# Kernel optimization log

Measured on AMD Instinct MI355X. Metric: run time of the kernel, lower is better.

## Reference

```python
import jax, jax.numpy as jnp
import numpy as np

D_MODEL, HEADS, GROUPS, DIM_HEAD = 256, 8, 8, 64
INNER = HEADS * DIM_HEAD              # 512
OFF_DIMS = INNER // GROUPS            # 64 channels fed to the offset network per group
DF, OFF_SCALE, KS, PAD = 4, 4.0, 6, 1  # downsample_factor, offset_scale, kernel, (6-4)//2
CPB_DIM = D_MODEL // 4                # 64
NUM_LAYERS = 6
SCALE = DIM_HEAD ** -0.5
B, H, W = 1, 40, 40


def grouped_conv1x1(x, w, g):
    # x: (b, cin, h, w); w: (cout, cin//g) torch grouped 1x1 conv weight (squeezed)
    b, cin, h, wd = x.shape
    cout = w.shape[0]
    xg = x.reshape(b, g, cin // g, h, wd)
    wg = w.reshape(g, cout // g, cin // g)
    return jnp.einsum('goi,bgihw->bgohw', wg, xg).reshape(b, cout, h, wd)


def create_grid(h, w, dtype):
    # torch meshgrid(arange(w), arange(h), indexing='xy') stacked at dim 0
    ys, xs = jnp.meshgrid(jnp.arange(h, dtype=dtype), jnp.arange(w, dtype=dtype), indexing='ij')
    return jnp.stack((xs, ys))  # (2, h, w): channel0 = x, channel1 = y


def normalize_grid(grid):
    # faithful to source: channel0 scaled by (h-1), channel1 by (w-1); out dim last
    h, w = grid.shape[-2:]
    g0 = 2.0 * grid[..., 0, :, :] / max(h - 1, 1) - 1.0
    g1 = 2.0 * grid[..., 1, :, :] / max(w - 1, 1) - 1.0
    return jnp.stack((g0, g1), axis=-1)


def grid_sample_bilinear(img, grid):
    # torch F.grid_sample, mode='bilinear', padding_mode='zeros', align_corners=False
    Bn, C, Hh, Ww = img.shape
    gx = ((grid[..., 0] + 1.0) * Ww - 1.0) * 0.5
    gy = ((grid[..., 1] + 1.0) * Hh - 1.0) * 0.5
    x0 = jnp.floor(gx)
    y0 = jnp.floor(gy)
    wx1 = gx - x0
    wy1 = gy - y0
    flat = img.reshape(Bn, C, Hh * Ww)

    def gather(xi, yi):
        valid = (xi >= 0) & (xi <= Ww - 1) & (yi >= 0) & (yi <= Hh - 1)
        xc = jnp.clip(xi, 0, Ww - 1).astype(jnp.int32)
        yc = jnp.clip(yi, 0, Hh - 1).astype(jnp.int32)
        idx = (yc * Ww + xc).reshape(Bn, 1, -1)
        vals = jnp.take_along_axis(flat, idx, axis=2).reshape(Bn, C, *xi.shape[1:])
        return vals * valid[:, None].astype(img.dtype)

    return (gather(x0, y0) * ((1 - wx1) * (1 - wy1))[:, None]
            + gather(x0 + 1, y0) * (wx1 * (1 - wy1))[:, None]
            + gather(x0, y0 + 1) * ((1 - wx1) * wy1)[:, None]
            + gather(x0 + 1, y0 + 1) * (wx1 * wy1)[:, None])


def deform_attn(x, wq, wk, wv, w_off1, b_off1, w_off2,
                cpb_w0, cpb_b0, cpb_w1, cpb_b1, cpb_w2, cpb_b2, w_out, b_out):
    b, c, Hh, Ww = x.shape
    bg = b * GROUPS
    q = grouped_conv1x1(x, wq, GROUPS)                      # (b, 512, H, W)
    qg = q.reshape(bg, OFF_DIMS, Hh, Ww)                    # group heads: (b g) d h w
    # offset network: depthwise 6x6 stride-4 conv -> GELU -> 1x1 -> tanh * scale
    off = jax.lax.conv_general_dilated(
        qg, w_off1, (DF, DF), ((PAD, PAD), (PAD, PAD)),
        dimension_numbers=('NCHW', 'OIHW', 'NCHW'), feature_group_count=OFF_DIMS)
    off = jax.nn.gelu(off + b_off1[None, :, None, None], approximate=False)
    off = jnp.tanh(jnp.einsum('oc,bchw->bohw', w_off2, off)) * OFF_SCALE  # (bg,2,h',w')
    hp, wp = off.shape[-2:]
    vgrid = create_grid(hp, wp, x.dtype)[None] + off
    vgrid_scaled = normalize_grid(vgrid)                    # (bg, h', w', 2)
    xg = x.reshape(bg, c // GROUPS, Hh, Ww)
    kv = grid_sample_bilinear(xg, vgrid_scaled).reshape(b, c, hp, wp)
    k = grouped_conv1x1(kv, wk, GROUPS)
    v = grouped_conv1x1(kv, wv, GROUPS)
    i, j = Hh * Ww, hp * wp
    qh = (q * SCALE).reshape(b, HEADS, DIM_HEAD, i).transpose(0, 1, 3, 2)  # bhid
    kh = k.reshape(b, HEADS, DIM_HEAD, j).transpose(0, 1, 3, 2)
    vh = v.reshape(b, HEADS, DIM_HEAD, j).transpose(0, 1, 3, 2)
    sim = jnp.einsum('bhid,bhjd->bhij', qh, kh)
    # continuous positional bias (CPB, depth-2 MLP on signed-log relative coords)
    grid_q = normalize_grid(create_grid(Hh, Ww, x.dtype)).reshape(i, 2)
    grid_kv = vgrid_scaled.reshape(bg, j, 2)
    pos = grid_q[None, :, None, :] - grid_kv[:, None, :, :]  # (bg, i, j, 2)
    bias = jnp.sign(pos) * jnp.log1p(jnp.abs(pos))
    bias = jax.nn.relu(bias @ cpb_w0.T + cpb_b0)
    bias = jax.nn.relu(bias @ cpb_w1.T + cpb_b1)
    bias = bias @ cpb_w2.T + cpb_b2                          # (bg, i, j, 1)
    sim = sim + bias.reshape(b, GROUPS, i, j)                # heads//offset_groups == 1
    attn = jax.nn.softmax(sim, axis=-1)                      # stable softmax (matches amax-subtract)
    out = jnp.einsum('bhij,bhjd->bhid', attn, vh)
    out = out.transpose(0, 1, 3, 2).reshape(b, INNER, Hh, Ww)
    return jnp.einsum('oc,bchw->bohw', w_out, out) + b_out[None, :, None, None]


def setup_inputs() -> dict:
    key = jax.random.key(0)
    ks = jax.random.split(key, 16)
    L = NUM_LAYERS

    def p(k, shape, scale=0.02):
        return jax.random.normal(k, shape, dtype=jnp.float32) * scale

    return {
        'bev_feat': jax.random.normal(ks[0], (B, D_MODEL, H, W), dtype=jnp.float32),
        'wq': p(ks[1], (L, INNER, D_MODEL // GROUPS)),
        'wk': p(ks[2], (L, INNER, D_MODEL // GROUPS)),
        'wv': p(ks[3], (L, INNER, D_MODEL // GROUPS)),
        'w_off1': p(ks[4], (L, OFF_DIMS, 1, KS, KS)),
        'b_off1': jnp.zeros((L, OFF_DIMS), jnp.float32),
        'w_off2': p(ks[5], (L, 2, OFF_DIMS)),
        'cpb_w0': p(ks[6], (L, CPB_DIM, 2), 0.5),
        'cpb_b0': jnp.zeros((L, CPB_DIM), jnp.float32),
        'cpb_w1': p(ks[7], (L, CPB_DIM, CPB_DIM), 0.1),
        'cpb_b1': jnp.zeros((L, CPB_DIM), jnp.float32),
        'cpb_w2': p(ks[8], (L, 1, CPB_DIM), 0.1),
        'cpb_b2': jnp.zeros((L, 1), jnp.float32),
        'w_out': p(ks[9], (L, D_MODEL, INNER)),
        'b_out': jnp.zeros((L, D_MODEL), jnp.float32),
    }


def reference(bev_feat, wq, wk, wv, w_off1, b_off1, w_off2,
              cpb_w0, cpb_b0, cpb_w1, cpb_b1, cpb_w2, cpb_b2, w_out, b_out):
    # The source encoder loop runs `output = layer(bev_feat)` on the ORIGINAL
    # input each iteration, so only the last layer's output survives. Faithful
    # math = apply layer NUM_LAYERS-1 once (dropout in eval mode -> identity).
    l = NUM_LAYERS - 1
    return deform_attn(bev_feat, wq[l], wk[l], wv[l], w_off1[l], b_off1[l], w_off2[l],
                       cpb_w0[l], cpb_b0[l], cpb_w1[l], cpb_b1[l], cpb_w2[l], cpb_b2[l],
                       w_out[l], b_out[l])
```

## Files before the change

### kernel.cpp

```cpp
#include <hip/hip_runtime.h>
#include <math.h>


#define NP 1600
#define NJ 100

typedef _Float16 f16x8 __attribute__((ext_vector_type(8)));
typedef _Float16 f16x4 __attribute__((ext_vector_type(4)));
typedef _Float16 f16x2 __attribute__((ext_vector_type(2)));
typedef float  f32x4  __attribute__((ext_vector_type(4)));
typedef float  f32x2  __attribute__((ext_vector_type(2)));

template<int CTRL>
__device__ __forceinline__ float dpp_add(float x) {
  int y = __builtin_amdgcn_update_dpp(0, __builtin_bit_cast(int, x),
                                      CTRL, 0xf, 0xf, true);
  return x + __builtin_bit_cast(float, y);
}

__global__ __launch_bounds__(256, 4) void k_off_cpb(
    const float* __restrict__ x, const float* __restrict__ wq,
    const float* __restrict__ wdw,
    const float* __restrict__ bdw, const float* __restrict__ wo2,
    const float* __restrict__ wk, const float* __restrict__ wv,
    const float* __restrict__ w0, const float* __restrict__ b0,
    const float* __restrict__ w1, const float* __restrict__ b1v,
    const float* __restrict__ cw2, const float* __restrict__ b2,
    float* __restrict__ kout, float* __restrict__ vout_t,
    _Float16* __restrict__ bias16) {
  __shared__ float x_lds[36][36];
  __shared__ float psum[4][72];
  __shared__ float su_l[40];
  __shared__ float sv_l[40];
  __shared__ _Float16 a16[40][72];
  __shared__ _Float16 c16[40][72];
  int b = blockIdx.x;
  int g = b & 7;
  int j = b >> 3;
  int gj = g * 100 + j;
  int t = threadIdx.x;
  int lane = t & 63;
  int wv_id = t >> 6;
  int oy = j / 10, ox = j - (j / 10) * 10;
  int row = lane & 15;
  int kgrp = lane >> 4;

  for (int idx = t; idx < 1152; idx += 256) {
    int ci = idx / 36, tap = idx - (idx / 36) * 36;
    int ky = tap / 6, kx = tap - (tap / 6) * 6;
    int iy = oy * 4 - 1 + ky;
    int ix = ox * 4 - 1 + kx;
    float v = 0.f;
    if (iy >= 0 && iy < 40 && ix >= 0 && ix < 40)
      v = x[(g * 32 + ci) * NP + iy * 40 + ix];
    x_lds[tap][ci] = v;
  }
  __syncthreads();

  {
    float wqreg[32];
    const float* wqr = wq + (size_t)(g * 64 + lane) * 32;
#pragma unroll
    for (int q4 = 0; q4 < 8; ++q4) {
      f32x4 a = *(const f32x4*)(wqr + q4 * 4);
#pragma unroll
      for (int e = 0; e < 4; ++e) wqreg[q4 * 4 + e] = a[e];
    }
    float acc = 0.f;
#pragma unroll
    for (int tu = 0; tu < 9; ++tu) {
      int tt = wv_id * 9 + tu;
      float qv = 0.f;
#pragma unroll
      for (int q4 = 0; q4 < 8; ++q4) {
        f32x4 xv = *(const f32x4*)&x_lds[tt][q4 * 4];
#pragma unroll
        for (int e = 0; e < 4; ++e)
          qv = fmaf(wqreg[q4 * 4 + e], xv[e], qv);
      }
      acc = fmaf(wdw[lane * 36 + tt], qv, acc);
    }
    psum[wv_id][lane] = acc;
  }
  __syncthreads();

  if (wv_id == 0) {
    float accd = psum[0][lane] + psum[1][lane] + psum[2][lane] + psum[3][lane]
               + bdw[lane];
    float od = 0.5f * accd * (1.0f + erff(accd * 0.70710678118654752440f));
    float px = wo2[lane] * od, py = wo2[64 + lane] * od;
#pragma unroll
    for (int m = 1; m < 64; m <<= 1) {
      px += __shfl_xor(px, m);
      py += __shfl_xor(py, m);
    }
    float ax = tanhf(px) * 4.f;
    float ay = tanhf(py) * 4.f;
    float vx = (float)ox + ax;
    float vy = (float)oy + ay;
    float g0 = 2.f * vx / 9.f - 1.f;
    float g1 = 2.f * vy / 9.f - 1.f;
    if (lane < 40) {
      float qc = (float)lane * (2.f / 39.f) - 1.f;
      float u = qc - g0;
      float vv2 = qc - g1;
      su_l[lane] = copysignf(log1pf(fabsf(u)), u);
      sv_l[lane] = copysignf(log1pf(fabsf(vv2)), vv2);
    }
    float gx = ((g0 + 1.f) * 40.f - 1.f) * 0.5f;
    float gy = ((g1 + 1.f) * 40.f - 1.f) * 0.5f;
    float x0f = floorf(gx), y0f = floorf(gy);
    float wx = gx - x0f, wy = gy - y0f;
    bool mx0 = (x0f >= 0.f) && (x0f <= 39.f);
    bool mx1 = (x0f + 1.f >= 0.f) && (x0f + 1.f <= 39.f);
    bool my0 = (y0f >= 0.f) && (y0f <= 39.f);
    bool my1 = (y0f + 1.f >= 0.f) && (y0f + 1.f <= 39.f);
    int ix0 = (int)fminf(fmaxf(x0f, 0.f), 39.f);
    int ix1 = (int)fminf(fmaxf(x0f + 1.f, 0.f), 39.f);
    int iy0 = (int)fminf(fmaxf(y0f, 0.f), 39.f);
    int iy1 = (int)fminf(fmaxf(y0f + 1.f, 0.f), 39.f);
    float w00 = (1.f - wx) * (1.f - wy) * ((mx0 && my0) ? 1.f : 0.f);
    float w10 = wx * (1.f - wy) * ((mx1 && my0) ? 1.f : 0.f);
    float w01 = (1.f - wx) * wy * ((mx0 && my1) ? 1.f : 0.f);
    float w11 = wx * wy * ((mx1 && my1) ? 1.f : 0.f);
    int b00 = iy0 * 40 + ix0, b10 = iy0 * 40 + ix1;
    int b01 = iy1 * 40 + ix0, b11 = iy1 * 40 + ix1;
    float kvc = 0.f;
    if (lane < 32) {
      const float* xc = x + (g * 32 + lane) * NP;
      kvc = w00 * xc[b00] + w10 * xc[b10] + w01 * xc[b01] + w11 * xc[b11];
    }
    const float* wkr = wk + (g * 64 + lane) * 32;
    const float* wvr = wv + (g * 64 + lane) * 32;
    float wkreg[32], wvreg[32];
#pragma unroll
    for (int q4 = 0; q4 < 8; ++q4) {
      f32x4 a = *(const f32x4*)(wkr + q4 * 4);
      f32x4 bq = *(const f32x4*)(wvr + q4 * 4);
#pragma unroll
      for (int e = 0; e < 4; ++e) { wkreg[q4 * 4 + e] = a[e]; wvreg[q4 * 4 + e] = bq[e]; }
    }
    float kacc = 0.f, vacc = 0.f;
#pragma unroll
    for (int c = 0; c < 32; ++c) {
      float kvb = __shfl(kvc, c);
      kacc = fmaf(wkreg[c], kvb, kacc);
      vacc = fmaf(wvreg[c], kvb, vacc);
    }
    kout[(g * 64 + lane) * 100 + j] = kacc;
    vout_t[(size_t)gj * 64 + lane] = vacc;
  }
  __syncthreads();

  for (int idx = t; idx < 2560; idx += 256) {
    int xi = idx >> 6, kk = idx & 63;
    a16[xi][kk] = (_Float16)fmaf(w0[2 * kk], su_l[xi], b0[kk]);
    c16[xi][kk] = (_Float16)(w0[2 * kk + 1] * sv_l[xi]);
  }

  f16x8 B[4][2];
#pragma unroll
  for (int ct = 0; ct < 4; ++ct)
#pragma unroll
    for (int s = 0; s < 2; ++s)
#pragma unroll
      for (int e = 0; e < 8; ++e)
        B[ct][s][e] = (_Float16)w1[(ct * 16 + row) * 64 + s * 32 + kgrp * 8 + e];
  float b1c[4], w2c[4];
#pragma unroll
  for (int ct = 0; ct < 4; ++ct) {
    b1c[ct] = b1v[ct * 16 + row];
    w2c[ct] = cw2[ct * 16 + row];
  }
  float bb = b2[0];
  _Float16* outp = bias16 + (size_t)gj * 1600;
  __syncthreads();

  int it0 = wv_id * 25;
  int iy = wv_id * 10;
  int ix = row;
  f16x8 zero8 = {};
  for (int it = it0; it < it0 + 25; ++it) {
    f32x4 acc[4];
#pragma unroll
    for (int ct = 0; ct < 4; ++ct) {
      acc[ct][0] = 0.f; acc[ct][1] = 0.f; acc[ct][2] = 0.f; acc[ct][3] = 0.f;
    }
#pragma unroll
    for (int s = 0; s < 2; ++s) {
      f16x8 av = *(const f16x8*)&a16[ix][s * 32 + kgrp * 8];
      f16x8 cv = *(const f16x8*)&c16[iy][s * 32 + kgrp * 8];
      f16x8 A = __builtin_elementwise_max(av + cv, zero8);
#pragma unroll
      for (int ct = 0; ct < 4; ++ct)
        acc[ct] = __builtin_amdgcn_mfma_f32_16x16x32_f16(A, B[ct][s], acc[ct], 0, 0, 0);
    }
    float part[4];
#pragma unroll
    for (int ri = 0; ri < 4; ++ri) {
      float s2 = 0.f;
#pragma unroll
      for (int ct = 0; ct < 4; ++ct) {
        float val = acc[ct][ri] + b1c[ct];
        s2 = fmaf(w2c[ct], fmaxf(val, 0.f), s2);
      }
      part[ri] = s2;
    }
#pragma unroll
    for (int ri = 0; ri < 4; ++ri) {
      part[ri] = dpp_add<0xB1>(part[ri]);
      part[ri] = dpp_add<0x4E>(part[ri]);
      part[ri] = dpp_add<0x141>(part[ri]);
      part[ri] = dpp_add<0x140>(part[ri]);
    }
    if (row == 0) {
      f16x4 o;
      o[0] = (_Float16)(part[0] + bb); o[1] = (_Float16)(part[1] + bb);
      o[2] = (_Float16)(part[2] + bb); o[3] = (_Float16)(part[3] + bb);
      *(f16x4*)(outp + it * 16 + kgrp * 4) = o;
    }
    ix += 16;
    if (ix >= 40) { ix -= 40; ++iy; }
  }
}

__global__ __launch_bounds__(256) void k_attn(
    const float* __restrict__ x, const float* __restrict__ wq,
    const float* __restrict__ k, const float* __restrict__ v_t,
    const _Float16* __restrict__ bias16, float* __restrict__ inner) {
  __shared__ float v_lds[100][68];
  __shared__ float s_lds[16][100];
  __shared__ float q_lds[64][20];
  __shared__ float x_tile[32][16];
  int h = blockIdx.x / 100;
  int i0 = (blockIdx.x - h * 100) * 16;
  int t = threadIdx.x;
  for (int idx = t; idx < 6400; idx += 256) {
    int j = idx >> 6, d = idx & 63;
    v_lds[j][d] = v_t[(size_t)h * 6400 + idx];
  }
  for (int idx = t; idx < 512; idx += 256) {
    int ci = idx >> 4, i = idx & 15;
    x_tile[ci][i] = x[(h * 32 + ci) * NP + i0 + i];
  }
  __syncthreads();
  {
    int d = t & 63;
    int i4 = t >> 6;
    f32x4 wr[8];
#pragma unroll
    for (int qq = 0; qq < 8; ++qq)
      wr[qq] = *(const f32x4*)(wq + (size_t)(h * 64 + d) * 32 + qq * 4);
#pragma unroll
    for (int ii = 0; ii < 4; ++ii) {
      int i = i4 * 4 + ii;
      float acc = 0.f;
#pragma unroll
      for (int ci = 0; ci < 32; ++ci)
        acc = fmaf(wr[ci >> 2][ci & 3], x_tile[ci][i], acc);
      q_lds[d][i] = acc;
    }
  }
  __syncthreads();
  if (t < 200) {
    int ib = (t / 25) * 2, jb = (t % 25) * 4;
    const float* kp = k + h * 64 * 100 + jb;
    float a[2][4];
#pragma unroll
    for (int ii = 0; ii < 2; ++ii)
#pragma unroll
      for (int jj = 0; jj < 4; ++jj) a[ii][jj] = 0.f;
#pragma unroll 8
    for (int d = 0; d < 64; ++d) {
      f32x2 qv = *(const f32x2*)&q_lds[d][ib];
      f32x4 kv4 = *(const f32x4*)(kp + d * 100);
#pragma unroll
      for (int ii = 0; ii < 2; ++ii)
#pragma unroll
        for (int jj = 0; jj < 4; ++jj)
          a[ii][jj] = fmaf(qv[ii], kv4[jj], a[ii][jj]);
    }
    const _Float16* bcol = bias16 + (size_t)h * 100 * 1600;
#pragma unroll
    for (int jj = 0; jj < 4; ++jj) {
      f16x2 bv = *(const f16x2*)(bcol + (size_t)(jb + jj) * 1600 + i0 + ib);
#pragma unroll
      for (int ii = 0; ii < 2; ++ii)
        s_lds[ib + ii][jb + jj] = fmaf(a[ii][jj], 0.125f, (float)bv[ii]);
    }
  }
  __syncthreads();
  {
    int i = t >> 4, sub = t & 15;
    float m = -1e30f;
    for (int j = sub; j < 100; j += 16) m = fmaxf(m, s_lds[i][j]);
#pragma unroll
    for (int off = 1; off < 16; off <<= 1) m = fmaxf(m, __shfl_xor(m, off));
    float sum = 0.f;
    for (int j = sub; j < 100; j += 16) {
      float e = expf(s_lds[i][j] - m);
      s_lds[i][j] = e;
      sum += e;
    }
#pragma unroll
    for (int off = 1; off < 16; off <<= 1) sum += __shfl_xor(sum, off);
    float inv = 1.f / sum;
    for (int j = sub; j < 100; j += 16) s_lds[i][j] *= inv;
  }
  __syncthreads();
  {
    int i = t & 15, db = (t >> 4) * 4;
    float acc[4];
#pragma unroll
    for (int dd = 0; dd < 4; ++dd) acc[dd] = 0.f;
    for (int jc = 0; jc < 25; ++jc) {
      f32x4 sv = *(const f32x4*)&s_lds[i][jc * 4];
#pragma unroll
      for (int jj = 0; jj < 4; ++jj) {
        f32x4 vv = *(const f32x4*)&v_lds[jc * 4 + jj][db];
#pragma unroll
        for (int dd = 0; dd < 4; ++dd)
          acc[dd] = fmaf(sv[jj], vv[dd], acc[dd]);
      }
    }
#pragma unroll
    for (int dd = 0; dd < 4; ++dd)
      inner[(h * 64 + db + dd) * NP + i0 + i] = acc[dd];
  }
}

__global__ __launch_bounds__(256) void k_proj(
    const float* __restrict__ inner, const float* __restrict__ w,
    const float* __restrict__ bo, float* __restrict__ out) {
  int oc = blockIdx.x & 31;
  int pt = blockIdx.x >> 5;
  int t = threadIdx.x;
  int quad = __builtin_amdgcn_readfirstlane(t >> 6);
  int o0 = oc * 8 + quad * 2;
  int p = pt * 64 + (t & 63);
  const float* w0r = w + (size_t)o0 * 512;
  float a0 = 0.f, a1 = 0.f;
#pragma unroll 8
  for (int c = 0; c < 512; ++c) {
    float xv = inner[c * NP + p];
    a0 = fmaf(w0r[c], xv, a0);
    a1 = fmaf(w0r[512 + c], xv, a1);
  }
  out[(o0 + 0) * NP + p] = a0 + bo[o0 + 0];
  out[(o0 + 1) * NP + p] = a1 + bo[o0 + 1];
}

extern "C" void kernel_launch(void* const* d_in, const int* in_sizes, int n_in,
                              void* d_out, int out_size, void* d_ws, size_t ws_size,
                              hipStream_t stream) {
  int L = in_sizes[1] / (512 * 32);
  int l = L - 1;
  const float* x      = (const float*)d_in[0];
  const float* wq     = (const float*)d_in[1]  + (size_t)l * 512 * 32;
  const float* wk     = (const float*)d_in[2]  + (size_t)l * 512 * 32;
  const float* wv     = (const float*)d_in[3]  + (size_t)l * 512 * 32;
  const float* w_off1 = (const float*)d_in[4]  + (size_t)l * 64 * 36;
  const float* b_off1 = (const float*)d_in[5]  + (size_t)l * 64;
  const float* w_off2 = (const float*)d_in[6]  + (size_t)l * 2 * 64;
  const float* cpb_w0 = (const float*)d_in[7]  + (size_t)l * 64 * 2;
  const float* cpb_b0 = (const float*)d_in[8]  + (size_t)l * 64;
  const float* cpb_w1 = (const float*)d_in[9]  + (size_t)l * 64 * 64;
  const float* cpb_b1 = (const float*)d_in[10] + (size_t)l * 64;
  const float* cpb_w2 = (const float*)d_in[11] + (size_t)l * 64;
  const float* cpb_b2 = (const float*)d_in[12] + (size_t)l * 1;
  const float* w_out  = (const float*)d_in[13] + (size_t)l * 256 * 512;
  const float* b_out  = (const float*)d_in[14] + (size_t)l * 256;
  float* out = (float*)d_out;

  float* ws = (float*)d_ws;
  float*    k_ws    = ws;
  float*    vt_ws   = ws + 51200;
  _Float16* bias16  = (_Float16*)(ws + 102400);
  float*    inner   = ws + 742400;

  k_off_cpb<<<800, 256, 0, stream>>>(x, wq, w_off1, b_off1, w_off2, wk, wv,
                                     cpb_w0, cpb_b0, cpb_w1, cpb_b1, cpb_w2,
                                     cpb_b2, k_ws, vt_ws, bias16);
  k_attn<<<800, 256, 0, stream>>>(x, wq, k_ws, vt_ws, bias16, inner);
  k_proj<<<800, 256, 0, stream>>>(inner, w_out, b_out, out);
}
```

Before: 91.89 us.

## Fuse output projection into attention kernel with per-head atomic accumulation

Removes the separate projection kernel and the global round-trip of the inner activation. Each attention block now stores its 16x64 head output in reused LDS, multiplies it by that head's 64-column slice of w_out, and atomically adds into a pre-zeroed output. Head 7 adds the bias. This trades one launch and the inner buffer traffic for a memset, 8-way float atomics per output element, and redundant weight reads from global memory in every block.

```diff
diff --git a/kernel.cpp b/kernel.cpp
--- a/kernel.cpp
+++ b/kernel.cpp
@@ -227,7 +227,9 @@
 __global__ __launch_bounds__(256) void k_attn(
     const float* __restrict__ x, const float* __restrict__ wq,
     const float* __restrict__ k, const float* __restrict__ v_t,
-    const _Float16* __restrict__ bias16, float* __restrict__ inner) {
+    const _Float16* __restrict__ bias16,
+    const float* __restrict__ wout, const float* __restrict__ bout,
+    float* __restrict__ out) {
   __shared__ float v_lds[100][68];
   __shared__ float s_lds[16][100];
   __shared__ float q_lds[64][20];
@@ -308,6 +310,7 @@
     for (int j = sub; j < 100; j += 16) s_lds[i][j] *= inv;
   }
   __syncthreads();
+  float (*inner_blk)[68] = (float(*)[68])&q_lds[0][0];
   {
     int i = t & 15, db = (t >> 4) * 4;
     float acc[4];
@@ -323,31 +326,39 @@
           acc[dd] = fmaf(sv[jj], vv[dd], acc[dd]);
       }
     }
-#pragma unroll
-    for (int dd = 0; dd < 4; ++dd)
-      inner[(h * 64 + db + dd) * NP + i0 + i] = acc[dd];
-  }
-}
-
-__global__ __launch_bounds__(256) void k_proj(
-    const float* __restrict__ inner, const float* __restrict__ w,
-    const float* __restrict__ bo, float* __restrict__ out) {
-  int oc = blockIdx.x & 31;
-  int pt = blockIdx.x >> 5;
-  int t = threadIdx.x;
-  int quad = __builtin_amdgcn_readfirstlane(t >> 6);
-  int o0 = oc * 8 + quad * 2;
-  int p = pt * 64 + (t & 63);
-  const float* w0r = w + (size_t)o0 * 512;
-  float a0 = 0.f, a1 = 0.f;
-#pragma unroll 8
-  for (int c = 0; c < 512; ++c) {
-    float xv = inner[c * NP + p];
-    a0 = fmaf(w0r[c], xv, a0);
-    a1 = fmaf(w0r[512 + c], xv, a1);
-  }
-  out[(o0 + 0) * NP + p] = a0 + bo[o0 + 0];
-  out[(o0 + 1) * NP + p] = a1 + bo[o0 + 1];
+    f32x4 o4;
+#pragma unroll
+    for (int dd = 0; dd < 4; ++dd) o4[dd] = acc[dd];
+    *(f32x4*)&inner_blk[i][db] = o4;
+  }
+  __syncthreads();
+  {
+    int o_grp = t >> 4, p_loc = t & 15;
+    int p = i0 + p_loc;
+    const float* ib = &inner_blk[p_loc][0];
+    float po[16];
+#pragma unroll
+    for (int oo = 0; oo < 16; ++oo) po[oo] = 0.f;
+#pragma unroll 4
+    for (int c4 = 0; c4 < 16; ++c4) {
+      f32x4 iv = *(const f32x4*)(ib + c4 * 4);
+#pragma unroll
+      for (int oo = 0; oo < 16; ++oo) {
+        f32x4 w4 = *(const f32x4*)(wout + (size_t)(o_grp * 16 + oo) * 512
+                                   + h * 64 + c4 * 4);
+#pragma unroll
+        for (int e = 0; e < 4; ++e)
+          po[oo] = fmaf(w4[e], iv[e], po[oo]);
+      }
+    }
+    if (h == 7) {
+#pragma unroll
+      for (int oo = 0; oo < 16; ++oo) po[oo] += bout[o_grp * 16 + oo];
+    }
+#pragma unroll
+    for (int oo = 0; oo < 16; ++oo)
+      atomicAdd(&out[(size_t)(o_grp * 16 + oo) * NP + p], po[oo]);
+  }
 }
 
 extern "C" void kernel_launch(void* const* d_in, const int* in_sizes, int n_in,
@@ -376,11 +387,11 @@
   float*    k_ws    = ws;
   float*    vt_ws   = ws + 51200;
   _Float16* bias16  = (_Float16*)(ws + 102400);
-  float*    inner   = ws + 742400;
-
+
+  hipMemsetAsync(out, 0, (size_t)out_size * sizeof(float), stream);
   k_off_cpb<<<800, 256, 0, stream>>>(x, wq, w_off1, b_off1, w_off2, wk, wv,
                                      cpb_w0, cpb_b0, cpb_w1, cpb_b1, cpb_w2,
                                      cpb_b2, k_ws, vt_ws, bias16);
-  k_attn<<<800, 256, 0, stream>>>(x, wq, k_ws, vt_ws, bias16, inner);
-  k_proj<<<800, 256, 0, stream>>>(inner, w_out, b_out, out);
+  k_attn<<<800, 256, 0, stream>>>(x, wq, k_ws, vt_ws, bias16,
+                                  w_out, b_out, out);
 }
```

Result: slower. 101.9 us (+10.9%).
